# Optimization experiments

Hardware: AMD Instinct MI355X
Metric: run time of the kernel (lower is better)

Reference implementation:

```python
import jax, jax.numpy as jnp
import numpy as np
import math

N = 20000          # real nodes (batch_size)
D = 256            # hidden_dim
H = 4              # num_heads
L = 3              # num_layers
E = 320000         # local edges
EXP_DEG = 4        # expander_degree
LN_EPS = 1e-5


def setup_inputs() -> dict:
    key = jax.random.key(0)
    ks = jax.random.split(key, 8)
    x = jax.random.normal(ks[0], (N, D), jnp.float32)
    rng = np.random.default_rng(0)
    edge_index = jnp.asarray(rng.integers(0, N, size=(2, E)), dtype=jnp.int32)
    # Expander: EXP_DEG//2 random permutations on N+1 nodes (incl. virtual node),
    # each contributing edges in both directions -> degree-EXP_DEG regular graph.
    n = N + 1
    perms = [rng.permutation(n) for _ in range(EXP_DEG // 2)]
    src = np.concatenate([np.arange(n) for _ in perms] + perms)
    dst = np.concatenate(perms + [np.arange(n) for _ in perms])
    exp_edge_index = jnp.asarray(np.stack([src, dst]), dtype=jnp.int32)
    s_in = 1.0 / math.sqrt(D)
    s_ffn = 1.0 / math.sqrt(4 * D)
    def w(k, shape, s):
        return jax.random.normal(k, shape, jnp.float32) * s
    params = {
        'Wqkv_loc': w(ks[1], (L, D, 3 * D), s_in), 'bqkv_loc': jnp.zeros((L, 3 * D), jnp.float32),
        'Wo_loc':   w(ks[2], (L, D, D), s_in),     'bo_loc':   jnp.zeros((L, D), jnp.float32),
        'Wqkv_exp': w(ks[3], (L, D, 3 * D), s_in), 'bqkv_exp': jnp.zeros((L, 3 * D), jnp.float32),
        'Wo_exp':   w(ks[4], (L, D, D), s_in),     'bo_exp':   jnp.zeros((L, D), jnp.float32),
        'ln_g': jnp.ones((L, D), jnp.float32),     'ln_b': jnp.zeros((L, D), jnp.float32),
        'W1': w(ks[5], (L, D, 4 * D), s_in),       'b1': jnp.zeros((L, 4 * D), jnp.float32),
        'W2': w(ks[6], (L, 4 * D, D), s_ffn),      'b2': jnp.zeros((L, D), jnp.float32),
    }
    return {'x': x, 'edge_index': edge_index, 'exp_edge_index': exp_edge_index, **params}


def _attention(h, src, dst, Wqkv, bqkv, Wo, bo):
    # Sparse multi-head attention over (src -> dst) edges with segment softmax per dst.
    n, d = h.shape
    dh = d // H
    qkv = (h @ Wqkv + bqkv).reshape(n, 3, H, dh)
    q, k, v = qkv[:, 0], qkv[:, 1], qkv[:, 2]            # [n, H, dh]
    score = (q[dst] * k[src]).sum(-1) / jnp.sqrt(jnp.float32(dh))  # [e, H]
    m = jax.ops.segment_max(score, dst, num_segments=n)  # [n, H]
    ex = jnp.exp(score - m[dst])
    denom = jax.ops.segment_sum(ex, dst, num_segments=n)
    alpha = ex / (denom[dst] + 1e-16)
    out = jax.ops.segment_sum(alpha[:, :, None] * v[src], dst, num_segments=n)  # [n, H, dh]
    return out.reshape(n, d) @ Wo + bo


def _layer_norm(x, g, b):
    mu = x.mean(-1, keepdims=True)
    var = ((x - mu) ** 2).mean(-1, keepdims=True)
    return (x - mu) * jax.lax.rsqrt(var + LN_EPS) * g + b


def reference(x, edge_index, exp_edge_index, Wqkv_loc, bqkv_loc, Wo_loc, bo_loc,
              Wqkv_exp, bqkv_exp, Wo_exp, bo_exp, ln_g, ln_b, W1, b1, W2, b2):
    n0 = x.shape[0]
    # VirtualNode transform: append one zero-feature node connected to/from all nodes.
    h = jnp.concatenate([x, jnp.zeros((1, x.shape[1]), x.dtype)], axis=0)
    ar = jnp.arange(n0, dtype=edge_index.dtype)
    vn = jnp.full((n0,), n0, dtype=edge_index.dtype)
    src = jnp.concatenate([edge_index[0], ar, vn])
    dst = jnp.concatenate([edge_index[1], vn, ar])
    esrc, edst = exp_edge_index[0], exp_edge_index[1]
    for l in range(L):  # fixed small number of structurally distinct layers
        res = h
        loc = _attention(h, src, dst, Wqkv_loc[l], bqkv_loc[l], Wo_loc[l], bo_loc[l])
        exp = _attention(h, esrc, edst, Wqkv_exp[l], bqkv_exp[l], Wo_exp[l], bo_exp[l])
        h = _layer_norm(res + loc + exp, ln_g[l], ln_b[l])
        h = h + (jax.nn.gelu(h @ W1[l] + b1[l], approximate=False) @ W2[l] + b2[l])
    return h[:n0]
```

## Files before the change

kernel.cpp:

```cpp
#include <hip/hip_runtime.h>
#include <stdint.h>

#define NREAL   20000
#define NNODES  20001
#define VN      20000
#define E_EDGES 320000
#define NEXP    80004
#define MPAD    20096
#define NVNW    320

typedef unsigned short u16;
typedef unsigned int   u32;
typedef __bf16 bf16x8 __attribute__((ext_vector_type(8)));
typedef float  f32x4  __attribute__((ext_vector_type(4)));
typedef u16    u16x8  __attribute__((ext_vector_type(8)));

__device__ __host__ __forceinline__ size_t fmoff(int row, int col, int LD) {
    return (size_t)(row >> 4) * ((size_t)LD * 16) + (size_t)((col >> 3) * 128)
         + (size_t)((row & 15) * 8) + (size_t)(col & 7);
}

__device__ __forceinline__ int qkv_perm(int n) {
    if (n < 256) return n;
    int u = n - 256;
    int part = u >> 8;
    int cl = u & 255;
    return 256 + (cl >> 2) * 8 + part * 4 + (cl & 3);
}

__device__ __forceinline__ float bf2f(u16 v) {
    union { u32 u; float f; } x; x.u = ((u32)v) << 16; return x.f;
}
__device__ __forceinline__ u16 f2bf(float f) {
    union { float f; u32 u; } x; x.f = f;
    u32 r = (x.u + 0x7fffu + ((x.u >> 16) & 1u)) >> 16;
    return (u16)r;
}
__device__ __forceinline__ float4 cvt4(ushort4 u) {
    return make_float4(bf2f(u.x), bf2f(u.y), bf2f(u.z), bf2f(u.w));
}
__device__ __forceinline__ float4 ld4bf(const u16* p) { return cvt4(*(const ushort4*)p); }
__device__ __forceinline__ float4 cvtk8(u16x8 r) {
    return make_float4(bf2f(r[0]), bf2f(r[1]), bf2f(r[2]), bf2f(r[3]));
}
__device__ __forceinline__ float4 cvtv8(u16x8 r) {
    return make_float4(bf2f(r[4]), bf2f(r[5]), bf2f(r[6]), bf2f(r[7]));
}


__global__ void hinit_kernel(const float* __restrict__ x, float* __restrict__ h,
                             u16* __restrict__ hb) {
    int idx = blockIdx.x * 256 + threadIdx.x;
    if (idx >= NNODES * 64) return;
    int row = idx >> 6, c0 = (idx & 63) * 4;
    float4 v = make_float4(0.f, 0.f, 0.f, 0.f);
    if (row < NREAL) v = *(const float4*)(x + (size_t)row * 256 + c0);
    *(float4*)(h + (size_t)row * 256 + c0) = v;
    ushort4 o;
    o.x = f2bf(v.x); o.y = f2bf(v.y); o.z = f2bf(v.z); o.w = f2bf(v.w);
    *(ushort4*)(hb + fmoff(row, c0, 256)) = o;
}

__global__ void init_kernel(int* cnt, int* fill, int* ecnt,
                            const float* __restrict__ bl, const float* __restrict__ be,
                            float* __restrict__ bcat,
                            const float* __restrict__ bol, const float* __restrict__ boe,
                            float* __restrict__ bsum) {
    int i = blockIdx.x * 256 + threadIdx.x;
    if (i < NREAL) { cnt[i] = 0; fill[i] = 0; }
    if (i < NNODES) ecnt[i] = 0;
    if (i < 3 * 1536) {
        int l = i / 1536, c = i - l * 1536;
        float v = (c < 768) ? bl[l * 768 + c] : be[l * 768 + c - 768];
        int cc = (c >= 768) ? c - 768 : c;
        int d = qkv_perm(cc) + ((c >= 768) ? 768 : 0);
        bcat[l * 1536 + d] = v;
    }
    if (i < 3 * 256) bsum[i] = bol[i] + boe[i];
}

__global__ void csr_count_kernel(const int* __restrict__ ei, int* __restrict__ cnt) {
    int e = blockIdx.x * 256 + threadIdx.x;
    if (e < E_EDGES) atomicAdd(&cnt[ei[E_EDGES + e]], 1);
}

__global__ void csr_scan_kernel(const int* __restrict__ cnt, int* __restrict__ indptr) {
    __shared__ int ssum[256];
    int t = threadIdx.x;
    int c0 = t * 79;
    int s = 0;
    for (int j = 0; j < 79; j++) {
        int i = c0 + j;
        if (i < NREAL) s += cnt[i];
    }
    ssum[t] = s;
    __syncthreads();
    for (int d2 = 1; d2 < 256; d2 <<= 1) {
        int v = (t >= d2) ? ssum[t - d2] : 0;
        __syncthreads();
        ssum[t] += v;
        __syncthreads();
    }
    int run = (t == 0) ? 0 : ssum[t - 1];
    for (int j = 0; j < 79; j++) {
        int i = c0 + j;
        if (i < NREAL) { indptr[i] = run; run += cnt[i]; }
    }
    if (t == 255) indptr[NREAL] = run;
}

__global__ void csr_scatter_kernel(const int* __restrict__ ei, const int* __restrict__ indptr,
                                   int* __restrict__ fill, int* __restrict__ srcs) {
    int e = blockIdx.x * 256 + threadIdx.x;
    if (e < E_EDGES) {
        int d = ei[E_EDGES + e];
        int pos = indptr[d] + atomicAdd(&fill[d], 1);
        srcs[pos] = ei[e];
    }
}

__global__ void exp_scatter_kernel(const int* __restrict__ eei, int* __restrict__ ecnt,
                                   int* __restrict__ esrcs) {
    int e = blockIdx.x * 256 + threadIdx.x;
    if (e < NEXP) {
        int d = eei[NEXP + e];
        int pos = atomicAdd(&ecnt[d], 1);
        esrcs[d * 4 + pos] = eei[e];
    }
}

__global__ void wconv_all_kernel(const float* __restrict__ WqkvL, const float* __restrict__ WqkvE,
                                 const float* __restrict__ WoL, const float* __restrict__ WoE,
                                 const float* __restrict__ W1, const float* __restrict__ W2,
                                 u16* __restrict__ out) {
    int i = blockIdx.x * 256 + threadIdx.x;
    if (i >= 3 * 1048576) return;
    int l = i / 1048576, r = i - l * 1048576;
    if (r >= 393216 && r < 524288) {
        int r2 = r - 393216;
        int k = r2 >> 8, n = r2 & 255;
        float v = (k < 256) ? WoL[(size_t)l * 65536 + k * 256 + n]
                            : WoE[(size_t)l * 65536 + (k - 256) * 256 + n];
        out[(size_t)l * 1048576 + 393216 + fmoff(n, k, 512)] = f2bf(v);
        return;
    }
    const float* src; int K, N; int base;
    if (r < 196608)      { src = WqkvL; K = 256;  N = 768;  base = 0; }
    else if (r < 393216) { src = WqkvE; K = 256;  N = 768;  base = 196608; }
    else if (r < 786432) { src = W1;    K = 256;  N = 1024; base = 524288; }
    else                 { src = W2;    K = 1024; N = 256;  base = 786432; }
    int r2 = r - base;
    int k = r2 / N, n = r2 - k * N;
    int d = (r < 393216) ? qkv_perm(n) : n;
    out[(size_t)l * 1048576 + base + fmoff(d, k, K)] = f2bf(src[(size_t)l * K * N + r2]);
}

__global__ __launch_bounds__(256) void qkv_rw(
    const u16* __restrict__ A, const u16* __restrict__ Bt, const float* __restrict__ bias,
    u16* __restrict__ Q0, u16* __restrict__ KV0,
    u16* __restrict__ Q1, u16* __restrict__ KV1, int M) {
    const int lin = blockIdx.x;
    const int mt = lin / 6, ns = lin - mt * 6;
    const int tm = mt * 64;
    if (tm >= M) return;
    const int tid = threadIdx.x;
    const int w = tid >> 6, lane = tid & 63;
    const int lm = lane & 15, q = lane >> 4;

    f32x4 acc[4][4];
#pragma unroll
    for (int a = 0; a < 4; a++)
#pragma unroll
        for (int b = 0; b < 4; b++) acc[a][b] = (f32x4)0.0f;

    const u16* apf[4];
    const u16* bpf[4];
#pragma unroll
    for (int mi = 0; mi < 4; mi++)
        apf[mi] = A + (size_t)(tm / 16 + mi) * 4096 + q * 128 + lm * 8;
#pragma unroll
    for (int ni = 0; ni < 4; ni++)
        bpf[ni] = Bt + (size_t)(ns * 16 + w * 4 + ni) * 4096 + q * 128 + lm * 8;

    bf16x8 sA[3][4], sB[3][4];
#pragma unroll
    for (int s = 0; s < 2; s++) {
#pragma unroll
        for (int mi = 0; mi < 4; mi++) sA[s][mi] = *(const bf16x8*)(apf[mi] + s * 512);
#pragma unroll
        for (int ni = 0; ni < 4; ni++) sB[s][ni] = *(const bf16x8*)(bpf[ni] + s * 512);
    }
#pragma unroll
    for (int i = 0; i < 8; i++) {
        const int cu = i % 3, pf = (i + 2) % 3;
        if (i + 2 < 8) {
#pragma unroll
            for (int mi = 0; mi < 4; mi++) sA[pf][mi] = *(const bf16x8*)(apf[mi] + (i + 2) * 512);
#pragma unroll
            for (int ni = 0; ni < 4; ni++) sB[pf][ni] = *(const bf16x8*)(bpf[ni] + (i + 2) * 512);
        }
#pragma unroll
        for (int mi = 0; mi < 4; mi++)
#pragma unroll
            for (int ni = 0; ni < 4; ni++)
                acc[mi][ni] = __builtin_amdgcn_mfma_f32_16x16x32_bf16(
                    sB[cu][ni], sA[cu][mi], acc[mi][ni], 0, 0, 0);
    }

    float4 b4[4];
#pragma unroll
    for (int ni = 0; ni < 4; ni++)
        b4[ni] = *(const float4*)(bias + ns * 256 + w * 64 + ni * 16 + q * 4);

#pragma unroll
    for (int mi = 0; mi < 4; mi++) {
        int grow = tm + mi * 16 + lm;
        if (grow >= M) continue;
#pragma unroll
        for (int ni = 0; ni < 4; ni++) {
            int gcol = ns * 256 + w * 64 + ni * 16 + q * 4;
            float v0 = acc[mi][ni][0] + b4[ni].x;
            float v1 = acc[mi][ni][1] + b4[ni].y;
            float v2 = acc[mi][ni][2] + b4[ni].z;
            float v3 = acc[mi][ni][3] + b4[ni].w;
            ushort4 o;
            o.x = f2bf(v0); o.y = f2bf(v1); o.z = f2bf(v2); o.w = f2bf(v3);
            u16* dst;
            if (gcol < 256)       dst = Q0  + (size_t)grow * 256 + gcol;
            else if (gcol < 768)  dst = KV0 + (size_t)grow * 512 + (gcol - 256);
            else if (gcol < 1024) dst = Q1  + (size_t)grow * 256 + (gcol - 768);
            else                  dst = KV1 + (size_t)grow * 512 + (gcol - 1024);
            *(ushort4*)dst = o;
        }
    }
}

__global__ __launch_bounds__(256) void ffn1_rw(
    const u16* __restrict__ A, const u16* __restrict__ Bt, const float* __restrict__ bias,
    u16* __restrict__ Cb, int M) {
    const int lin = blockIdx.x;
    const int mt = lin >> 2, ns = lin & 3;
    const int tm = mt * 64;
    if (tm >= M) return;
    const int tid = threadIdx.x;
    const int w = tid >> 6, lane = tid & 63;
    const int lm = lane & 15, q = lane >> 4;

    f32x4 acc[4][4];
#pragma unroll
    for (int a = 0; a < 4; a++)
#pragma unroll
        for (int b = 0; b < 4; b++) acc[a][b] = (f32x4)0.0f;

    const u16* apf[4];
    const u16* bpf[4];
#pragma unroll
    for (int mi = 0; mi < 4; mi++)
        apf[mi] = A + (size_t)(tm / 16 + mi) * 4096 + q * 128 + lm * 8;
#pragma unroll
    for (int ni = 0; ni < 4; ni++)
        bpf[ni] = Bt + (size_t)(ns * 16 + w * 4 + ni) * 4096 + q * 128 + lm * 8;

    bf16x8 sA[3][4], sB[3][4];
#pragma unroll
    for (int s = 0; s < 2; s++) {
#pragma unroll
        for (int mi = 0; mi < 4; mi++) sA[s][mi] = *(const bf16x8*)(apf[mi] + s * 512);
#pragma unroll
        for (int ni = 0; ni < 4; ni++) sB[s][ni] = *(const bf16x8*)(bpf[ni] + s * 512);
    }
#pragma unroll
    for (int i = 0; i < 8; i++) {
        const int cu = i % 3, pf = (i + 2) % 3;
        if (i + 2 < 8) {
#pragma unroll
            for (int mi = 0; mi < 4; mi++) sA[pf][mi] = *(const bf16x8*)(apf[mi] + (i + 2) * 512);
#pragma unroll
            for (int ni = 0; ni < 4; ni++) sB[pf][ni] = *(const bf16x8*)(bpf[ni] + (i + 2) * 512);
        }
#pragma unroll
        for (int mi = 0; mi < 4; mi++)
#pragma unroll
            for (int ni = 0; ni < 4; ni++)
                acc[mi][ni] = __builtin_amdgcn_mfma_f32_16x16x32_bf16(
                    sB[cu][ni], sA[cu][mi], acc[mi][ni], 0, 0, 0);
    }

    float4 b4[4];
#pragma unroll
    for (int ni = 0; ni < 4; ni++)
        b4[ni] = *(const float4*)(bias + ns * 256 + w * 64 + ni * 16 + q * 4);

#pragma unroll
    for (int mi = 0; mi < 4; mi++) {
        int grow = tm + mi * 16 + lm;
        if (grow >= M) continue;
#pragma unroll
        for (int ni = 0; ni < 4; ni++) {
            int gcol = ns * 256 + w * 64 + ni * 16 + q * 4;
            float v0 = acc[mi][ni][0] + b4[ni].x;
            float v1 = acc[mi][ni][1] + b4[ni].y;
            float v2 = acc[mi][ni][2] + b4[ni].z;
            float v3 = acc[mi][ni][3] + b4[ni].w;
            float g0, g1, g2, g3;
            {
                float u = 0.7978845608f * (v0 + 0.044715f * v0 * v0 * v0);
                g0 = 0.5f * v0 * (2.0f - 2.0f / (__expf(2.0f * u) + 1.0f));
            }
            {
                float u = 0.7978845608f * (v1 + 0.044715f * v1 * v1 * v1);
                g1 = 0.5f * v1 * (2.0f - 2.0f / (__expf(2.0f * u) + 1.0f));
            }
            {
                float u = 0.7978845608f * (v2 + 0.044715f * v2 * v2 * v2);
                g2 = 0.5f * v2 * (2.0f - 2.0f / (__expf(2.0f * u) + 1.0f));
            }
            {
                float u = 0.7978845608f * (v3 + 0.044715f * v3 * v3 * v3);
                g3 = 0.5f * v3 * (2.0f - 2.0f / (__expf(2.0f * u) + 1.0f));
            }
            ushort4 o;
            o.x = f2bf(g0); o.y = f2bf(g1); o.z = f2bf(g2); o.w = f2bf(g3);
            *(ushort4*)(Cb + fmoff(grow, gcol, 1024)) = o;
        }
    }
}

__global__ __launch_bounds__(256) void wo_ln_rw(
    const u16* __restrict__ A, const u16* __restrict__ Bt, const float* __restrict__ bias,
    const float* __restrict__ resid, const float* __restrict__ g,
    const float* __restrict__ bvec, float* __restrict__ hout, u16* __restrict__ hb,
    int M) {
    __shared__ float smS[32][4];
    __shared__ float smQ[32][4];
    const int tm = blockIdx.x * 32;
    if (tm >= M) return;
    const int tid = threadIdx.x;
    const int w = tid >> 6, lane = tid & 63;
    const int lm = lane & 15, q = lane >> 4;

    f32x4 acc[2][4];
#pragma unroll
    for (int a = 0; a < 2; a++)
#pragma unroll
        for (int b = 0; b < 4; b++) acc[a][b] = (f32x4)0.0f;

    const u16* apf[2];
    const u16* bpf[4];
#pragma unroll
    for (int mi = 0; mi < 2; mi++)
        apf[mi] = A + (size_t)(tm / 16 + mi) * 8192 + q * 128 + lm * 8;
#pragma unroll
    for (int ni = 0; ni < 4; ni++)
        bpf[ni] = Bt + (size_t)(w * 4 + ni) * 8192 + q * 128 + lm * 8;

    bf16x8 sA[3][2], sB[3][4];
#pragma unroll
    for (int s = 0; s < 2; s++) {
#pragma unroll
        for (int mi = 0; mi < 2; mi++) sA[s][mi] = *(const bf16x8*)(apf[mi] + s * 512);
#pragma unroll
        for (int ni = 0; ni < 4; ni++) sB[s][ni] = *(const bf16x8*)(bpf[ni] + s * 512);
    }
#pragma unroll
    for (int i = 0; i < 16; i++) {
        const int cu = i % 3, pf = (i + 2) % 3;
        if (i + 2 < 16) {
#pragma unroll
            for (int mi = 0; mi < 2; mi++) sA[pf][mi] = *(const bf16x8*)(apf[mi] + (i + 2) * 512);
#pragma unroll
            for (int ni = 0; ni < 4; ni++) sB[pf][ni] = *(const bf16x8*)(bpf[ni] + (i + 2) * 512);
        }
#pragma unroll
        for (int mi = 0; mi < 2; mi++)
#pragma unroll
            for (int ni = 0; ni < 4; ni++)
                acc[mi][ni] = __builtin_amdgcn_mfma_f32_16x16x32_bf16(
                    sB[cu][ni], sA[cu][mi], acc[mi][ni], 0, 0, 0);
    }

    float4 b4[4];
#pragma unroll
    for (int ni = 0; ni < 4; ni++)
        b4[ni] = *(const float4*)(bias + w * 64 + ni * 16 + q * 4);
#pragma unroll
    for (int mi = 0; mi < 2; mi++) {
        int grow = tm + mi * 16 + lm;
#pragma unroll
        for (int ni = 0; ni < 4; ni++) {
            int gcol = w * 64 + ni * 16 + q * 4;
            size_t idx = (size_t)grow * 256 + gcol;
            float4 rv = *(const float4*)(resid + idx);
            acc[mi][ni][0] = rv.x + (acc[mi][ni][0] + b4[ni].x);
            acc[mi][ni][1] = rv.y + (acc[mi][ni][1] + b4[ni].y);
            acc[mi][ni][2] = rv.z + (acc[mi][ni][2] + b4[ni].z);
            acc[mi][ni][3] = rv.w + (acc[mi][ni][3] + b4[ni].w);
        }
    }

    float s1[2];
#pragma unroll
    for (int mi = 0; mi < 2; mi++) {
        float s = 0.f;
#pragma unroll
        for (int ni = 0; ni < 4; ni++)
            s += acc[mi][ni][0] + acc[mi][ni][1] + acc[mi][ni][2] + acc[mi][ni][3];
        s += __shfl_xor(s, 16); s += __shfl_xor(s, 32);
        s1[mi] = s;
    }
    if (lane < 16) {
        smS[lm][w] = s1[0];
        smS[16 + lm][w] = s1[1];
    }
    __syncthreads();
    float mu[2];
#pragma unroll
    for (int mi = 0; mi < 2; mi++) {
        int r = mi * 16 + lm;
        mu[mi] = (smS[r][0] + smS[r][1] + smS[r][2] + smS[r][3]) * (1.0f / 256.0f);
    }
    float s2[2];
#pragma unroll
    for (int mi = 0; mi < 2; mi++) {
        float s = 0.f;
#pragma unroll
        for (int ni = 0; ni < 4; ni++) {
            float d0 = acc[mi][ni][0] - mu[mi];
            float d1 = acc[mi][ni][1] - mu[mi];
            float d2 = acc[mi][ni][2] - mu[mi];
            float d3 = acc[mi][ni][3] - mu[mi];
            s += d0 * d0 + d1 * d1 + d2 * d2 + d3 * d3;
        }
        s += __shfl_xor(s, 16); s += __shfl_xor(s, 32);
        s2[mi] = s;
    }
    if (lane < 16) {
        smQ[lm][w] = s2[0];
        smQ[16 + lm][w] = s2[1];
    }
    __syncthreads();
    float rinv[2];
#pragma unroll
    for (int mi = 0; mi < 2; mi++) {
        int r = mi * 16 + lm;
        float var = (smQ[r][0] + smQ[r][1] + smQ[r][2] + smQ[r][3]) * (1.0f / 256.0f);
        rinv[mi] = 1.0f / sqrtf(var + 1e-5f);
    }
#pragma unroll
    for (int mi = 0; mi < 2; mi++) {
        int grow = tm + mi * 16 + lm;
        if (grow >= M) continue;
#pragma unroll
        for (int ni = 0; ni < 4; ni++) {
            int gcol = w * 64 + ni * 16 + q * 4;
            float4 gv = *(const float4*)(g + gcol);
            float4 bv = *(const float4*)(bvec + gcol);
            float4 y;
            y.x = (acc[mi][ni][0] - mu[mi]) * rinv[mi] * gv.x + bv.x;
            y.y = (acc[mi][ni][1] - mu[mi]) * rinv[mi] * gv.y + bv.y;
            y.z = (acc[mi][ni][2] - mu[mi]) * rinv[mi] * gv.z + bv.z;
            y.w = (acc[mi][ni][3] - mu[mi]) * rinv[mi] * gv.w + bv.w;
            *(float4*)(hout + (size_t)grow * 256 + gcol) = y;
            ushort4 o;
            o.x = f2bf(y.x); o.y = f2bf(y.y); o.z = f2bf(y.z); o.w = f2bf(y.w);
            *(ushort4*)(hb + fmoff(grow, gcol, 256)) = o;
        }
    }
}

__global__ __launch_bounds__(256) void w2_rw(
    const u16* __restrict__ A, const u16* __restrict__ Bt, const float* __restrict__ bias,
    const float* __restrict__ resid, float* __restrict__ Cf, u16* __restrict__ Cb,
    int last, int M) {
    const int tm = blockIdx.x * 32;
    if (tm >= M) return;
    const int tid = threadIdx.x;
    const int w = tid >> 6, lane = tid & 63;
    const int lm = lane & 15, q = lane >> 4;

    f32x4 acc[2][4];
#pragma unroll
    for (int a = 0; a < 2; a++)
#pragma unroll
        for (int b = 0; b < 4; b++) acc[a][b] = (f32x4)0.0f;

    const u16* apf[2];
    const u16* bpf[4];
#pragma unroll
    for (int mi = 0; mi < 2; mi++)
        apf[mi] = A + (size_t)(tm / 16 + mi) * 16384 + q * 128 + lm * 8;
#pragma unroll
    for (int ni = 0; ni < 4; ni++)
        bpf[ni] = Bt + (size_t)(w * 4 + ni) * 16384 + q * 128 + lm * 8;

    bf16x8 sA[3][2], sB[3][4];
#pragma unroll
    for (int s = 0; s < 2; s++) {
#pragma unroll
        for (int mi = 0; mi < 2; mi++) sA[s][mi] = *(const bf16x8*)(apf[mi] + s * 512);
#pragma unroll
        for (int ni = 0; ni < 4; ni++) sB[s][ni] = *(const bf16x8*)(bpf[ni] + s * 512);
    }
#pragma unroll
    for (int i = 0; i < 32; i++) {
        const int cu = i % 3, pf = (i + 2) % 3;
        if (i + 2 < 32) {
#pragma unroll
            for (int mi = 0; mi < 2; mi++) sA[pf][mi] = *(const bf16x8*)(apf[mi] + (i + 2) * 512);
#pragma unroll
            for (int ni = 0; ni < 4; ni++) sB[pf][ni] = *(const bf16x8*)(bpf[ni] + (i + 2) * 512);
        }
#pragma unroll
        for (int mi = 0; mi < 2; mi++)
#pragma unroll
            for (int ni = 0; ni < 4; ni++)
                acc[mi][ni] = __builtin_amdgcn_mfma_f32_16x16x32_bf16(
                    sB[cu][ni], sA[cu][mi], acc[mi][ni], 0, 0, 0);
    }

    float4 b4[4];
#pragma unroll
    for (int ni = 0; ni < 4; ni++)
        b4[ni] = *(const float4*)(bias + w * 64 + ni * 16 + q * 4);

#pragma unroll
    for (int mi = 0; mi < 2; mi++) {
        int grow = tm + mi * 16 + lm;
        if (grow >= (last ? NREAL : M)) continue;
#pragma unroll
        for (int ni = 0; ni < 4; ni++) {
            int gcol = w * 64 + ni * 16 + q * 4;
            float v0 = acc[mi][ni][0] + b4[ni].x;
            float v1 = acc[mi][ni][1] + b4[ni].y;
            float v2 = acc[mi][ni][2] + b4[ni].z;
            float v3 = acc[mi][ni][3] + b4[ni].w;
            size_t idx = (size_t)grow * 256 + gcol;
            float4 rv = *(const float4*)(resid + idx);
            float o0 = rv.x + v0, o1 = rv.y + v1, o2 = rv.z + v2, o3 = rv.w + v3;
            *(float4*)(Cf + idx) = make_float4(o0, o1, o2, o3);
            if (!last) {
                ushort4 o;
                o.x = f2bf(o0); o.y = f2bf(o1); o.z = f2bf(o2); o.w = f2bf(o3);
                *(ushort4*)(Cb + fmoff(grow, gcol, 256)) = o;
            }
        }
    }
}

__global__ void vn_merge_kernel(const float* __restrict__ part, u16* __restrict__ acat) {
    __shared__ float sm[4][64][6];
    int w = threadIdx.x >> 6, lane = threadIdx.x & 63;
    int h = lane >> 4;
    int off = (h << 6) + (lane & 15) * 4;
    float M = -1e30f, L = 0.0f;
    float ax = 0, ay = 0, az = 0, aw = 0;
    for (int p = w * 80; p < w * 80 + 80; p++) {
        const float* pp = part + (size_t)p * 264;
        float pm = pp[h], pl = pp[4 + h];
        float4 nm = *(const float4*)(pp + 8 + off);
        float Mn = fmaxf(M, pm);
        float s0 = __expf(M - Mn);
        float s1 = __expf(pm - Mn);
        ax = ax * s0 + nm.x * s1;
        ay = ay * s0 + nm.y * s1;
        az = az * s0 + nm.z * s1;
        aw = aw * s0 + nm.w * s1;
        L = L * s0 + pl * s1;
        M = Mn;
    }
    sm[w][lane][0] = M; sm[w][lane][1] = L;
    sm[w][lane][2] = ax; sm[w][lane][3] = ay;
    sm[w][lane][4] = az; sm[w][lane][5] = aw;
    __syncthreads();
    if (w == 0) {
        float M2 = -1e30f, L2 = 0.0f;
        float bx = 0, by = 0, bz = 0, bw = 0;
#pragma unroll
        for (int p = 0; p < 4; p++) {
            float pm = sm[p][lane][0], pl = sm[p][lane][1];
            float Mn = fmaxf(M2, pm);
            float s0 = __expf(M2 - Mn);
            float s1 = __expf(pm - Mn);
            bx = bx * s0 + sm[p][lane][2] * s1;
            by = by * s0 + sm[p][lane][3] * s1;
            bz = bz * s0 + sm[p][lane][4] * s1;
            bw = bw * s0 + sm[p][lane][5] * s1;
            L2 = L2 * s0 + pl * s1;
            M2 = Mn;
        }
        float inv = 1.0f / (L2 + 1e-16f);
        ushort4 o;
        o.x = f2bf(bx * inv); o.y = f2bf(by * inv);
        o.z = f2bf(bz * inv); o.w = f2bf(bw * inv);
        *(ushort4*)(acat + fmoff(VN, off, 512)) = o;
    }
}

__global__ void attn_fused_kernel(const u16* __restrict__ qb_loc, const u16* __restrict__ kv_loc,
                                  const u16* __restrict__ qb_exp, const u16* __restrict__ kv_exp,
                                  const int* __restrict__ indptr, const int* __restrict__ srcs,
                                  const int* __restrict__ esrcs,
                                  u16* __restrict__ acat, float* __restrict__ part) {
    int gw0 = (int)((blockIdx.x * (size_t)blockDim.x + threadIdx.x) >> 6);
    int gw = __builtin_amdgcn_readfirstlane(gw0);
    int lane = threadIdx.x & 63;
    int h = lane >> 4;
    int off = (h << 6) + (lane & 15) * 4;
    int coff = (off >> 2) * 8;

    if (gw < NVNW) {
        int wv = gw;
        float4 qv = ld4bf(qb_loc + (size_t)VN * 256 + off);
        float m = -1e30f, l = 0.0f;
        float ax = 0, ay = 0, az = 0, aw = 0;
        for (int i = wv; i < NREAL; i += NVNW) {
            u16x8 r = *(const u16x8*)(kv_loc + (size_t)i * 512 + coff);
            float4 k4 = cvtk8(r);
            float4 v4 = cvtv8(r);
            float s = qv.x * k4.x + qv.y * k4.y + qv.z * k4.z + qv.w * k4.w;
            s += __shfl_xor(s, 1); s += __shfl_xor(s, 2);
            s += __shfl_xor(s, 4); s += __shfl_xor(s, 8);
            float sc = s * 0.125f;
            float mn = fmaxf(m, sc);
            float fold = __expf(m - mn);
            float ee = __expf(sc - mn);
            ax = ax * fold + v4.x * ee;
            ay = ay * fold + v4.y * ee;
            az = az * fold + v4.z * ee;
            aw = aw * fold + v4.w * ee;
            l = l * fold + ee;
            m = mn;
        }
        float* pp = part + (size_t)wv * 264;
        if ((lane & 15) == 0) { pp[h] = m; pp[4 + h] = l; }
        *(float4*)(pp + 8 + off) = make_float4(ax, ay, az, aw);
        return;
    }
    gw -= NVNW;

    const u16 *qb, *kv;
    const int* sl;
    int node, beg, deg, tot, cbase;
    if (gw < NREAL) {
        node = gw; qb = qb_loc; kv = kv_loc; sl = srcs; cbase = 0;
        beg = indptr[node]; deg = indptr[node + 1] - beg; tot = deg + 1;
    } else if (gw < NREAL + NNODES) {
        node = gw - NREAL;
        qb = qb_exp; kv = kv_exp; sl = esrcs; cbase = 256;
        beg = node * 4; deg = 4; tot = 4;
    } else {
        return;
    }

    float4 qv = ld4bf(qb + (size_t)node * 256 + off);
    float m = -1e30f, l = 0.0f;
    float ax = 0, ay = 0, az = 0, aw = 0;

    if (tot <= 4) {
        u16x8 raw[4];
#pragma unroll
        for (int j = 0; j < 4; j++) {
            int s = (j < deg) ? sl[beg + j] : VN;
            raw[j] = *(const u16x8*)(kv + (size_t)s * 512 + coff);
        }
        float sc[4];
#pragma unroll
        for (int j = 0; j < 4; j++) {
            float4 k4 = cvtk8(raw[j]);
            float p = qv.x * k4.x + qv.y * k4.y + qv.z * k4.z + qv.w * k4.w;
            p += __shfl_xor(p, 1); p += __shfl_xor(p, 2);
            p += __shfl_xor(p, 4); p += __shfl_xor(p, 8);
            sc[j] = (j < tot) ? p * 0.125f : -1e30f;
        }
        float mn = fmaxf(fmaxf(sc[0], sc[1]), fmaxf(sc[2], sc[3]));
#pragma unroll
        for (int j = 0; j < 4; j++) {
            float ee = __expf(sc[j] - mn);
            float4 v4 = cvtv8(raw[j]);
            ax += v4.x * ee; ay += v4.y * ee; az += v4.z * ee; aw += v4.w * ee;
            l += ee;
        }
        m = mn;
    } else {
        const int nch = (tot + 7) >> 3;
        u16x8 rA[8], rB[8];
#pragma unroll
        for (int j = 0; j < 8; j++) {
            int s = (j < deg) ? sl[beg + j] : VN;
            rA[j] = *(const u16x8*)(kv + (size_t)s * 512 + coff);
        }
        for (int c = 0; c < nch; c++) {
            if (c + 1 < nch) {
                const int e0n = (c + 1) * 8;
#pragma unroll
                for (int j = 0; j < 8; j++) {
                    int e = e0n + j;
                    int s = (e < deg) ? sl[beg + e] : VN;
                    rB[j] = *(const u16x8*)(kv + (size_t)s * 512 + coff);
                }
            }
            const int e0 = c * 8;
            float sc[8];
#pragma unroll
            for (int j = 0; j < 8; j++) {
                float4 k4 = cvtk8(rA[j]);
                float p = qv.x * k4.x + qv.y * k4.y + qv.z * k4.z + qv.w * k4.w;
                p += __shfl_xor(p, 1); p += __shfl_xor(p, 2);
                p += __shfl_xor(p, 4); p += __shfl_xor(p, 8);
                sc[j] = (e0 + j < tot) ? p * 0.125f : -1e30f;
            }
            float cmax = fmaxf(fmaxf(fmaxf(sc[0], sc[1]), fmaxf(sc[2], sc[3])),
                               fmaxf(fmaxf(sc[4], sc[5]), fmaxf(sc[6], sc[7])));
            float mn = fmaxf(m, cmax);
            float fold = __expf(m - mn);
            ax *= fold; ay *= fold; az *= fold; aw *= fold; l *= fold;
#pragma unroll
            for (int j = 0; j < 8; j++) {
                float ee = __expf(sc[j] - mn);
                float4 v4 = cvtv8(rA[j]);
                ax += v4.x * ee; ay += v4.y * ee; az += v4.z * ee; aw += v4.w * ee;
                l += ee;
            }
            m = mn;
#pragma unroll
            for (int j = 0; j < 8; j++) rA[j] = rB[j];
        }
    }
    float inv = 1.0f / (l + 1e-16f);
    ushort4 o;
    o.x = f2bf(ax * inv); o.y = f2bf(ay * inv);
    o.z = f2bf(az * inv); o.w = f2bf(aw * inv);
    *(ushort4*)(acat + fmoff(node, cbase + off, 512)) = o;
}


extern "C" void kernel_launch(void* const* d_in, const int* in_sizes, int n_in,
                              void* d_out, int out_size, void* d_ws, size_t ws_size,
                              hipStream_t stream) {
    (void)in_sizes; (void)n_in; (void)out_size;
    const float* x        = (const float*)d_in[0];
    const int*   ei       = (const int*)d_in[1];
    const int*   eei      = (const int*)d_in[2];
    const float* Wqkv_loc = (const float*)d_in[3];
    const float* bqkv_loc = (const float*)d_in[4];
    const float* Wo_loc   = (const float*)d_in[5];
    const float* bo_loc   = (const float*)d_in[6];
    const float* Wqkv_exp = (const float*)d_in[7];
    const float* bqkv_exp = (const float*)d_in[8];
    const float* Wo_exp   = (const float*)d_in[9];
    const float* bo_exp   = (const float*)d_in[10];
    const float* ln_g     = (const float*)d_in[11];
    const float* ln_b     = (const float*)d_in[12];
    const float* W1       = (const float*)d_in[13];
    const float* b1       = (const float*)d_in[14];
    const float* W2       = (const float*)d_in[15];
    const float* b2       = (const float*)d_in[16];

    char* wsp = (char*)d_ws;
    size_t off = 0;
    auto carve = [&](size_t bytes) -> void* {
        void* p = wsp + off;
        off += (bytes + 255) & ~(size_t)255;
        return p;
    };
    float* h_f    = (float*)carve((size_t)NNODES * 256 * 4);
    u16*   h_b    = (u16*)carve((size_t)MPAD * 256 * 2);
    u16*   qb_loc = (u16*)carve((size_t)NNODES * 256 * 2);
    u16*   kv_loc = (u16*)carve((size_t)NNODES * 512 * 2);
    u16*   qb_exp = (u16*)carve((size_t)NNODES * 256 * 2);
    u16*   kv_exp = (u16*)carve((size_t)NNODES * 512 * 2);
    u16*   acat   = (u16*)carve((size_t)MPAD * 512 * 2);
    u16*   wbf    = (u16*)carve((size_t)3 * 1048576 * 2);
    float* bcat   = (float*)carve((size_t)3 * 1536 * 4);
    float* bsum   = (float*)carve((size_t)3 * 256 * 4);
    int*   cnt    = (int*)carve((size_t)NREAL * 4);
    int*   indptr = (int*)carve((size_t)(NREAL + 1) * 4);
    int*   fill   = (int*)carve((size_t)NREAL * 4);
    int*   srcs   = (int*)carve((size_t)E_EDGES * 4);
    int*   ecnt   = (int*)carve((size_t)NNODES * 4);
    int*   esrcs  = (int*)carve((size_t)NNODES * 4 * 4);
    float* part   = (float*)carve((size_t)NVNW * 264 * 4);
    u16*   mid_d  = (u16*)carve((size_t)MPAD * 1024 * 2);
    u16*   mid    = (ws_size >= off) ? mid_d : qb_loc;

    hinit_kernel<<<(NNODES * 64 + 255) / 256, 256, 0, stream>>>(x, h_f, h_b);
    init_kernel<<<(NNODES + 255) / 256, 256, 0, stream>>>(
        cnt, fill, ecnt, bqkv_loc, bqkv_exp, bcat, bo_loc, bo_exp, bsum);
    csr_count_kernel<<<(E_EDGES + 255) / 256, 256, 0, stream>>>(ei, cnt);
    csr_scan_kernel<<<1, 256, 0, stream>>>(cnt, indptr);
    csr_scatter_kernel<<<(E_EDGES + 255) / 256, 256, 0, stream>>>(ei, indptr, fill, srcs);
    exp_scatter_kernel<<<(NEXP + 255) / 256, 256, 0, stream>>>(eei, ecnt, esrcs);
    wconv_all_kernel<<<(3 * 1048576 + 255) / 256, 256, 0, stream>>>(
        Wqkv_loc, Wqkv_exp, Wo_loc, Wo_exp, W1, W2, wbf);

    const int ATTN_BLOCKS = (NVNW + NREAL + NNODES + 3) / 4;
    const int QKV_BLOCKS = (MPAD / 64) * 6;
    const int RW32_BLOCKS = MPAD / 32;

    for (int l = 0; l < 3; l++) {
        const u16* wqkvC = wbf + (size_t)l * 1048576 + 0;
        const u16* wocat = wbf + (size_t)l * 1048576 + 393216;
        const u16* w1T   = wbf + (size_t)l * 1048576 + 524288;
        const u16* w2T   = wbf + (size_t)l * 1048576 + 786432;

        qkv_rw<<<QKV_BLOCKS, 256, 0, stream>>>(
            h_b, wqkvC, bcat + l * 1536,
            qb_loc, kv_loc, qb_exp, kv_exp, NNODES);

        attn_fused_kernel<<<ATTN_BLOCKS, 256, 0, stream>>>(
            qb_loc, kv_loc, qb_exp, kv_exp, indptr, srcs, esrcs, acat, part);
        vn_merge_kernel<<<1, 256, 0, stream>>>(part, acat);

        wo_ln_rw<<<RW32_BLOCKS, 256, 0, stream>>>(
            acat, wocat, bsum + l * 256, h_f,
            ln_g + l * 256, ln_b + l * 256, h_f, h_b, NNODES);

        ffn1_rw<<<320 * 4, 256, 0, stream>>>(
            h_b, w1T, b1 + l * 1024, mid, NNODES);

        if (l < 2) {
            w2_rw<<<RW32_BLOCKS, 256, 0, stream>>>(
                mid, w2T, b2 + l * 256, h_f, h_f, h_b, 0, NNODES);
        } else {
            w2_rw<<<RW32_BLOCKS, 256, 0, stream>>>(
                mid, w2T, b2 + l * 256, h_f, (float*)d_out, nullptr, 1, NNODES);
        }
    }
}
```

Before: 793.7 us.

## Fuse virtual-node merge into Wo/LN GEMM, halve QKV/FFN1 row tiles, deepen prefetch

The separate single-block vn_merge kernel is removed. Its partial-softmax merge for the virtual node now runs inside the wo_ln_rw block that owns row VN, before that block's GEMM. This saves one launch per layer, but that block does extra serial work first. The QKV and FFN1 GEMMs switch from 64-row to 32-row tiles, doubling block count for more occupancy and parallelism. All GEMMs deepen register prefetch from 2 to 3 stages, which raises register pressure.

Measured after the change: 766.4 us, median of 2. 3.4% less time.

```diff
diff --git a/kernel.cpp b/kernel.cpp
--- a/kernel.cpp
+++ b/kernel.cpp
@@ -161,46 +161,46 @@
     u16* __restrict__ Q1, u16* __restrict__ KV1, int M) {
     const int lin = blockIdx.x;
     const int mt = lin / 6, ns = lin - mt * 6;
-    const int tm = mt * 64;
+    const int tm = mt * 32;
     if (tm >= M) return;
     const int tid = threadIdx.x;
     const int w = tid >> 6, lane = tid & 63;
     const int lm = lane & 15, q = lane >> 4;
 
-    f32x4 acc[4][4];
-#pragma unroll
-    for (int a = 0; a < 4; a++)
+    f32x4 acc[2][4];
+#pragma unroll
+    for (int a = 0; a < 2; a++)
 #pragma unroll
         for (int b = 0; b < 4; b++) acc[a][b] = (f32x4)0.0f;
 
-    const u16* apf[4];
+    const u16* apf[2];
     const u16* bpf[4];
 #pragma unroll
-    for (int mi = 0; mi < 4; mi++)
+    for (int mi = 0; mi < 2; mi++)
         apf[mi] = A + (size_t)(tm / 16 + mi) * 4096 + q * 128 + lm * 8;
 #pragma unroll
     for (int ni = 0; ni < 4; ni++)
         bpf[ni] = Bt + (size_t)(ns * 16 + w * 4 + ni) * 4096 + q * 128 + lm * 8;
 
-    bf16x8 sA[3][4], sB[3][4];
-#pragma unroll
-    for (int s = 0; s < 2; s++) {
-#pragma unroll
-        for (int mi = 0; mi < 4; mi++) sA[s][mi] = *(const bf16x8*)(apf[mi] + s * 512);
+    bf16x8 sA[4][2], sB[4][4];
+#pragma unroll
+    for (int s = 0; s < 3; s++) {
+#pragma unroll
+        for (int mi = 0; mi < 2; mi++) sA[s][mi] = *(const bf16x8*)(apf[mi] + s * 512);
 #pragma unroll
         for (int ni = 0; ni < 4; ni++) sB[s][ni] = *(const bf16x8*)(bpf[ni] + s * 512);
     }
 #pragma unroll
     for (int i = 0; i < 8; i++) {
-        const int cu = i % 3, pf = (i + 2) % 3;
-        if (i + 2 < 8) {
-#pragma unroll
-            for (int mi = 0; mi < 4; mi++) sA[pf][mi] = *(const bf16x8*)(apf[mi] + (i + 2) * 512);
-#pragma unroll
-            for (int ni = 0; ni < 4; ni++) sB[pf][ni] = *(const bf16x8*)(bpf[ni] + (i + 2) * 512);
-        }
-#pragma unroll
-        for (int mi = 0; mi < 4; mi++)
+        const int cu = i & 3, pf = (i + 3) & 3;
+        if (i + 3 < 8) {
+#pragma unroll
+            for (int mi = 0; mi < 2; mi++) sA[pf][mi] = *(const bf16x8*)(apf[mi] + (i + 3) * 512);
+#pragma unroll
+            for (int ni = 0; ni < 4; ni++) sB[pf][ni] = *(const bf16x8*)(bpf[ni] + (i + 3) * 512);
+        }
+#pragma unroll
+        for (int mi = 0; mi < 2; mi++)
 #pragma unroll
             for (int ni = 0; ni < 4; ni++)
                 acc[mi][ni] = __builtin_amdgcn_mfma_f32_16x16x32_bf16(
@@ -213,7 +213,7 @@
         b4[ni] = *(const float4*)(bias + ns * 256 + w * 64 + ni * 16 + q * 4);
 
 #pragma unroll
-    for (int mi = 0; mi < 4; mi++) {
+    for (int mi = 0; mi < 2; mi++) {
         int grow = tm + mi * 16 + lm;
         if (grow >= M) continue;
 #pragma unroll
@@ -240,46 +240,46 @@
     u16* __restrict__ Cb, int M) {
     const int lin = blockIdx.x;
     const int mt = lin >> 2, ns = lin & 3;
-    const int tm = mt * 64;
+    const int tm = mt * 32;
     if (tm >= M) return;
     const int tid = threadIdx.x;
     const int w = tid >> 6, lane = tid & 63;
     const int lm = lane & 15, q = lane >> 4;
 
-    f32x4 acc[4][4];
-#pragma unroll
-    for (int a = 0; a < 4; a++)
+    f32x4 acc[2][4];
+#pragma unroll
+    for (int a = 0; a < 2; a++)
 #pragma unroll
         for (int b = 0; b < 4; b++) acc[a][b] = (f32x4)0.0f;
 
-    const u16* apf[4];
+    const u16* apf[2];
     const u16* bpf[4];
 #pragma unroll
-    for (int mi = 0; mi < 4; mi++)
+    for (int mi = 0; mi < 2; mi++)
         apf[mi] = A + (size_t)(tm / 16 + mi) * 4096 + q * 128 + lm * 8;
 #pragma unroll
     for (int ni = 0; ni < 4; ni++)
         bpf[ni] = Bt + (size_t)(ns * 16 + w * 4 + ni) * 4096 + q * 128 + lm * 8;
 
-    bf16x8 sA[3][4], sB[3][4];
-#pragma unroll
-    for (int s = 0; s < 2; s++) {
-#pragma unroll
-        for (int mi = 0; mi < 4; mi++) sA[s][mi] = *(const bf16x8*)(apf[mi] + s * 512);
+    bf16x8 sA[4][2], sB[4][4];
+#pragma unroll
+    for (int s = 0; s < 3; s++) {
+#pragma unroll
+        for (int mi = 0; mi < 2; mi++) sA[s][mi] = *(const bf16x8*)(apf[mi] + s * 512);
 #pragma unroll
         for (int ni = 0; ni < 4; ni++) sB[s][ni] = *(const bf16x8*)(bpf[ni] + s * 512);
     }
 #pragma unroll
     for (int i = 0; i < 8; i++) {
-        const int cu = i % 3, pf = (i + 2) % 3;
-        if (i + 2 < 8) {
-#pragma unroll
-            for (int mi = 0; mi < 4; mi++) sA[pf][mi] = *(const bf16x8*)(apf[mi] + (i + 2) * 512);
-#pragma unroll
-            for (int ni = 0; ni < 4; ni++) sB[pf][ni] = *(const bf16x8*)(bpf[ni] + (i + 2) * 512);
-        }
-#pragma unroll
-        for (int mi = 0; mi < 4; mi++)
+        const int cu = i & 3, pf = (i + 3) & 3;
+        if (i + 3 < 8) {
+#pragma unroll
+            for (int mi = 0; mi < 2; mi++) sA[pf][mi] = *(const bf16x8*)(apf[mi] + (i + 3) * 512);
+#pragma unroll
+            for (int ni = 0; ni < 4; ni++) sB[pf][ni] = *(const bf16x8*)(bpf[ni] + (i + 3) * 512);
+        }
+#pragma unroll
+        for (int mi = 0; mi < 2; mi++)
 #pragma unroll
             for (int ni = 0; ni < 4; ni++)
                 acc[mi][ni] = __builtin_amdgcn_mfma_f32_16x16x32_bf16(
@@ -292,7 +292,7 @@
         b4[ni] = *(const float4*)(bias + ns * 256 + w * 64 + ni * 16 + q * 4);
 
 #pragma unroll
-    for (int mi = 0; mi < 4; mi++) {
+    for (int mi = 0; mi < 2; mi++) {
         int grow = tm + mi * 16 + lm;
         if (grow >= M) continue;
 #pragma unroll
@@ -327,10 +327,10 @@
 }
 
 __global__ __launch_bounds__(256) void wo_ln_rw(
-    const u16* __restrict__ A, const u16* __restrict__ Bt, const float* __restrict__ bias,
+    const u16* A, const u16* __restrict__ Bt, const float* __restrict__ bias,
     const float* __restrict__ resid, const float* __restrict__ g,
     const float* __restrict__ bvec, float* __restrict__ hout, u16* __restrict__ hb,
-    int M) {
+    const float* __restrict__ part, u16* acat_w, int M) {
     __shared__ float smS[32][4];
     __shared__ float smQ[32][4];
     const int tm = blockIdx.x * 32;
@@ -339,6 +339,55 @@
     const int w = tid >> 6, lane = tid & 63;
     const int lm = lane & 15, q = lane >> 4;
 
+    if (blockIdx.x == VN / 32) {
+        __shared__ float smm[4][64][6];
+        int hh = lane >> 4;
+        int ov = (hh << 6) + (lane & 15) * 4;
+        float mm = -1e30f, ll = 0.0f;
+        float ax = 0, ay = 0, az = 0, aw = 0;
+        for (int p = w * 80; p < w * 80 + 80; p++) {
+            const float* pp = part + (size_t)p * 264;
+            float pm = pp[hh], pl = pp[4 + hh];
+            float4 nm = *(const float4*)(pp + 8 + ov);
+            float Mn = fmaxf(mm, pm);
+            float s0 = __expf(mm - Mn);
+            float s1 = __expf(pm - Mn);
+            ax = ax * s0 + nm.x * s1;
+            ay = ay * s0 + nm.y * s1;
+            az = az * s0 + nm.z * s1;
+            aw = aw * s0 + nm.w * s1;
+            ll = ll * s0 + pl * s1;
+            mm = Mn;
+        }
+        smm[w][lane][0] = mm; smm[w][lane][1] = ll;
+        smm[w][lane][2] = ax; smm[w][lane][3] = ay;
+        smm[w][lane][4] = az; smm[w][lane][5] = aw;
+        __syncthreads();
+        if (w == 0) {
+            float M2 = -1e30f, L2 = 0.0f;
+            float bx = 0, by = 0, bz = 0, bw = 0;
+#pragma unroll
+            for (int p = 0; p < 4; p++) {
+                float pm = smm[p][lane][0], pl = smm[p][lane][1];
+                float Mn = fmaxf(M2, pm);
+                float s0 = __expf(M2 - Mn);
+                float s1 = __expf(pm - Mn);
+                bx = bx * s0 + smm[p][lane][2] * s1;
+                by = by * s0 + smm[p][lane][3] * s1;
+                bz = bz * s0 + smm[p][lane][4] * s1;
+                bw = bw * s0 + smm[p][lane][5] * s1;
+                L2 = L2 * s0 + pl * s1;
+                M2 = Mn;
+            }
+            float inv = 1.0f / (L2 + 1e-16f);
+            ushort4 o;
+            o.x = f2bf(bx * inv); o.y = f2bf(by * inv);
+            o.z = f2bf(bz * inv); o.w = f2bf(bw * inv);
+            *(ushort4*)(acat_w + fmoff(VN, ov, 512)) = o;
+        }
+        __syncthreads();
+    }
+
     f32x4 acc[2][4];
 #pragma unroll
     for (int a = 0; a < 2; a++)
@@ -354,9 +403,9 @@
     for (int ni = 0; ni < 4; ni++)
         bpf[ni] = Bt + (size_t)(w * 4 + ni) * 8192 + q * 128 + lm * 8;
 
-    bf16x8 sA[3][2], sB[3][4];
-#pragma unroll
-    for (int s = 0; s < 2; s++) {
+    bf16x8 sA[4][2], sB[4][4];
+#pragma unroll
+    for (int s = 0; s < 3; s++) {
 #pragma unroll
         for (int mi = 0; mi < 2; mi++) sA[s][mi] = *(const bf16x8*)(apf[mi] + s * 512);
 #pragma unroll
@@ -364,12 +413,12 @@
     }
 #pragma unroll
     for (int i = 0; i < 16; i++) {
-        const int cu = i % 3, pf = (i + 2) % 3;
-        if (i + 2 < 16) {
-#pragma unroll
-            for (int mi = 0; mi < 2; mi++) sA[pf][mi] = *(const bf16x8*)(apf[mi] + (i + 2) * 512);
-#pragma unroll
-            for (int ni = 0; ni < 4; ni++) sB[pf][ni] = *(const bf16x8*)(bpf[ni] + (i + 2) * 512);
+        const int cu = i & 3, pf = (i + 3) & 3;
+        if (i + 3 < 16) {
+#pragma unroll
+            for (int mi = 0; mi < 2; mi++) sA[pf][mi] = *(const bf16x8*)(apf[mi] + (i + 3) * 512);
+#pragma unroll
+            for (int ni = 0; ni < 4; ni++) sB[pf][ni] = *(const bf16x8*)(bpf[ni] + (i + 3) * 512);
         }
 #pragma unroll
         for (int mi = 0; mi < 2; mi++)
@@ -493,9 +542,9 @@
     for (int ni = 0; ni < 4; ni++)
         bpf[ni] = Bt + (size_t)(w * 4 + ni) * 16384 + q * 128 + lm * 8;
 
-    bf16x8 sA[3][2], sB[3][4];
-#pragma unroll
-    for (int s = 0; s < 2; s++) {
+    bf16x8 sA[4][2], sB[4][4];
+#pragma unroll
+    for (int s = 0; s < 3; s++) {
 #pragma unroll
         for (int mi = 0; mi < 2; mi++) sA[s][mi] = *(const bf16x8*)(apf[mi] + s * 512);
 #pragma unroll
@@ -503,12 +552,12 @@
     }
 #pragma unroll
     for (int i = 0; i < 32; i++) {
-        const int cu = i % 3, pf = (i + 2) % 3;
-        if (i + 2 < 32) {
-#pragma unroll
-            for (int mi = 0; mi < 2; mi++) sA[pf][mi] = *(const bf16x8*)(apf[mi] + (i + 2) * 512);
-#pragma unroll
-            for (int ni = 0; ni < 4; ni++) sB[pf][ni] = *(const bf16x8*)(bpf[ni] + (i + 2) * 512);
+        const int cu = i & 3, pf = (i + 3) & 3;
+        if (i + 3 < 32) {
+#pragma unroll
+            for (int mi = 0; mi < 2; mi++) sA[pf][mi] = *(const bf16x8*)(apf[mi] + (i + 3) * 512);
+#pragma unroll
+            for (int ni = 0; ni < 4; ni++) sB[pf][ni] = *(const bf16x8*)(bpf[ni] + (i + 3) * 512);
         }
 #pragma unroll
         for (int mi = 0; mi < 2; mi++)
@@ -544,55 +593,6 @@
                 *(ushort4*)(Cb + fmoff(grow, gcol, 256)) = o;
             }
         }
-    }
-}
-
-__global__ void vn_merge_kernel(const float* __restrict__ part, u16* __restrict__ acat) {
-    __shared__ float sm[4][64][6];
-    int w = threadIdx.x >> 6, lane = threadIdx.x & 63;
-    int h = lane >> 4;
-    int off = (h << 6) + (lane & 15) * 4;
-    float M = -1e30f, L = 0.0f;
-    float ax = 0, ay = 0, az = 0, aw = 0;
-    for (int p = w * 80; p < w * 80 + 80; p++) {
-        const float* pp = part + (size_t)p * 264;
-        float pm = pp[h], pl = pp[4 + h];
-        float4 nm = *(const float4*)(pp + 8 + off);
-        float Mn = fmaxf(M, pm);
-        float s0 = __expf(M - Mn);
-        float s1 = __expf(pm - Mn);
-        ax = ax * s0 + nm.x * s1;
-        ay = ay * s0 + nm.y * s1;
-        az = az * s0 + nm.z * s1;
-        aw = aw * s0 + nm.w * s1;
-        L = L * s0 + pl * s1;
-        M = Mn;
-    }
-    sm[w][lane][0] = M; sm[w][lane][1] = L;
-    sm[w][lane][2] = ax; sm[w][lane][3] = ay;
-    sm[w][lane][4] = az; sm[w][lane][5] = aw;
-    __syncthreads();
-    if (w == 0) {
-        float M2 = -1e30f, L2 = 0.0f;
-        float bx = 0, by = 0, bz = 0, bw = 0;
-#pragma unroll
-        for (int p = 0; p < 4; p++) {
-            float pm = sm[p][lane][0], pl = sm[p][lane][1];
-            float Mn = fmaxf(M2, pm);
-            float s0 = __expf(M2 - Mn);
-            float s1 = __expf(pm - Mn);
-            bx = bx * s0 + sm[p][lane][2] * s1;
-            by = by * s0 + sm[p][lane][3] * s1;
-            bz = bz * s0 + sm[p][lane][4] * s1;
-            bw = bw * s0 + sm[p][lane][5] * s1;
-            L2 = L2 * s0 + pl * s1;
-            M2 = Mn;
-        }
-        float inv = 1.0f / (L2 + 1e-16f);
-        ushort4 o;
-        o.x = f2bf(bx * inv); o.y = f2bf(by * inv);
-        o.z = f2bf(bz * inv); o.w = f2bf(bw * inv);
-        *(ushort4*)(acat + fmoff(VN, off, 512)) = o;
     }
 }
 
@@ -794,8 +794,9 @@
         Wqkv_loc, Wqkv_exp, Wo_loc, Wo_exp, W1, W2, wbf);
 
     const int ATTN_BLOCKS = (NVNW + NREAL + NNODES + 3) / 4;
-    const int QKV_BLOCKS = (MPAD / 64) * 6;
     const int RW32_BLOCKS = MPAD / 32;
+    const int QKV_BLOCKS  = RW32_BLOCKS * 6;
+    const int FFN1_BLOCKS = RW32_BLOCKS * 4;
 
     for (int l = 0; l < 3; l++) {
         const u16* wqkvC = wbf + (size_t)l * 1048576 + 0;
@@ -809,13 +810,12 @@
 
         attn_fused_kernel<<<ATTN_BLOCKS, 256, 0, stream>>>(
             qb_loc, kv_loc, qb_exp, kv_exp, indptr, srcs, esrcs, acat, part);
-        vn_merge_kernel<<<1, 256, 0, stream>>>(part, acat);
 
         wo_ln_rw<<<RW32_BLOCKS, 256, 0, stream>>>(
             acat, wocat, bsum + l * 256, h_f,
-            ln_g + l * 256, ln_b + l * 256, h_f, h_b, NNODES);
-
-        ffn1_rw<<<320 * 4, 256, 0, stream>>>(
+            ln_g + l * 256, ln_b + l * 256, h_f, h_b, part, acat, NNODES);
+
+        ffn1_rw<<<FFN1_BLOCKS, 256, 0, stream>>>(
             h_b, w1T, b1 + l * 1024, mid, NNODES);
 
         if (l < 2) {
```
